# Kernel optimization log

Measured on AMD Instinct MI355X. Metric: run time of the kernel, lower is better.

Reference implementation:

```python
import jax, jax.numpy as jnp
import numpy as np
from jax import lax

M_POINT = 1024
NSAMPLE = 16
GRASPNESS_THRESHOLD = 0.1
HMIN, HMAX = -0.02, 0.04  # cylinder height range (GraspNet CloudCrop)
RADII = (0.025, 0.05, 0.075, 0.1)
BIG = 1e10


def _fps(xyz, mask):
    """Masked furthest point sampling. xyz [N,3], mask [N] bool -> idx [M_POINT] int32.
    Masked-out points carry -BIG min-distance so they are never selected."""
    first = jnp.argmax(mask).astype(jnp.int32)  # first graspable point (ragged FPS start)
    dists = jnp.where(mask, BIG, -BIG)
    idxs = jnp.zeros((M_POINT,), jnp.int32).at[0].set(first)

    def body(i, carry):
        idxs, dists = carry
        last = xyz[idxs[i - 1]]
        d = jnp.sum((xyz - last) ** 2, axis=-1)
        dists = jnp.where(mask, jnp.minimum(dists, d), -BIG)
        nxt = jnp.argmax(dists).astype(jnp.int32)
        return idxs.at[i].set(nxt), dists

    idxs, _ = lax.fori_loop(1, M_POINT, body, (idxs, dists))
    return idxs


def _cylinder_crop(xyz_g, feat_g, rot, radius, w1, b1, w2, b2):
    """Cylinder query + group + shared MLP + maxpool.
    xyz_g [B,M,3], feat_g [B,M,C], rot [B,M,3,3] -> [B,M,256]."""
    B, M, _ = xyz_g.shape
    # offsets of candidate n relative to seed m, expressed in the seed's gripper frame
    diff = xyz_g[:, None, :, :] - xyz_g[:, :, None, :]          # [B,M(seed),M(cand),3]
    local = jnp.einsum('bmnj,bmji->bmni', diff, rot)            # rotate into approach frame
    along = local[..., 0]
    r2 = local[..., 1] ** 2 + local[..., 2] ** 2
    cond = (r2 < radius * radius) & (along > HMIN) & (along < HMAX)  # [B,M,M]
    # first NSAMPLE in-cylinder indices (ball-query semantics: pad with first hit)
    order = jnp.where(cond, jnp.arange(M)[None, None, :], M)
    sel = jnp.argsort(order, axis=-1)[..., :NSAMPLE].astype(jnp.int32)  # [B,M,NS]
    cnt = cond.sum(axis=-1)                                     # [B,M]
    fill = sel[..., :1]
    idx = jnp.where(jnp.arange(NSAMPLE)[None, None, :] < cnt[..., None], sel, fill)
    idx = jnp.where(cnt[..., None] > 0, idx, 0)
    grouped_xyz = jnp.take_along_axis(local, idx[..., None], axis=2) / radius  # [B,M,NS,3]
    grouped_feat = feat_g[jnp.arange(B)[:, None, None], idx]                    # [B,M,NS,C]
    g = jnp.concatenate([grouped_xyz, grouped_feat], axis=-1)                   # [B,M,NS,3+C]
    h = jax.nn.relu(jnp.einsum('bmnf,of->bmno', g, w1) + b1)
    h = jax.nn.relu(jnp.einsum('bmnf,of->bmno', h, w2) + b2)
    return h.max(axis=2)                                                        # [B,M,256]


def setup_inputs() -> dict:
    key = jax.random.key(0)
    ks = jax.random.split(key, 10)
    B, N, C = 4, 20000, 512
    return {
        'seed_xyz': jax.random.normal(ks[0], (B, N, 3), jnp.float32),
        'seed_features': jax.random.normal(ks[1], (B, C, N), jnp.float32),
        'objectness_score': jax.random.normal(ks[2], (B, 2, N), jnp.float32),
        'graspness_score': jax.random.uniform(ks[3], (B, N), jnp.float32),
        'grasp_top_views_rot': jax.random.normal(ks[4], (B, M_POINT, 3, 3), jnp.float32),
        'crop_w1': jax.random.normal(ks[5], (4, 256, 3 + C), jnp.float32) * 0.05,
        'crop_b1': jnp.zeros((4, 256), jnp.float32),
        'crop_w2': jax.random.normal(ks[6], (4, 256, 256), jnp.float32) * 0.05,
        'crop_b2': jnp.zeros((4, 256), jnp.float32),
        'fuse_w': jax.random.normal(ks[7], (256, 1024), jnp.float32) * 0.05,
        'fuse_b': jnp.zeros((256,), jnp.float32),
    }


def reference(seed_xyz, seed_features, objectness_score, graspness_score,
              grasp_top_views_rot, crop_w1, crop_b1, crop_w2, crop_b2,
              fuse_w, fuse_b):
    # graspable mask (per-point, data dependent)
    objectness_mask = jnp.argmax(objectness_score, axis=1) == 1       # [B,N]
    graspness_mask = graspness_score > GRASPNESS_THRESHOLD
    graspable_mask = objectness_mask & graspness_mask
    # masked FPS per sample, then gather
    idxs = jax.vmap(_fps)(seed_xyz, graspable_mask)                    # [B,M]
    xyz_g = jnp.take_along_axis(seed_xyz, idxs[:, :, None], axis=1)    # [B,M,3]
    feat = seed_features.transpose(0, 2, 1)                            # [B,N,C]
    feat_g = jnp.take_along_axis(feat, idxs[:, :, None], axis=1)       # [B,M,C]
    # multiscale cylinder crops
    feats = [_cylinder_crop(xyz_g, feat_g, grasp_top_views_rot, RADII[k],
                            crop_w1[k], crop_b1[k], crop_w2[k], crop_b2[k])
             for k in range(4)]
    cat = jnp.concatenate(feats, axis=-1)                              # [B,M,1024]
    fused = jnp.einsum('bmf,of->bom', cat, fuse_w) + fuse_b[None, :, None]  # [B,256,M]
    return fused
```

## Files before the change

### kernel.cpp

```cpp
#include <hip/hip_runtime.h>
#include <cstdint>
#include <cfloat>
#include <climits>

#define NPTS 20000
#define NB 4
#define MP 1024
#define CF 512
#define MAXCH 20
#define PFIX 10
#define KFAST 10240
#define NWORK 8
#define PPT 20

__constant__ float c_r2[4]  = { (float)(0.025*0.025), (float)(0.05*0.05),
                                (float)(0.075*0.075), (float)(0.1*0.1) };
__constant__ float c_rad[4] = { 0.025f, 0.05f, 0.075f, 0.1f };

#define DPP_XOR1   0xB1
#define DPP_XOR2   0x4E
#define DPP_HMIRR  0x141
#define DPP_MIRR   0x140
#define DPP_BC15   0x142
#define DPP_BC31   0x143

template<int CTRL>
__device__ __forceinline__ unsigned long long kmax_step(unsigned long long k)
{
    unsigned int lo = (unsigned int)k;
    unsigned int hi = (unsigned int)(k >> 32);
    unsigned int olo = (unsigned int)__builtin_amdgcn_update_dpp((int)lo, (int)lo, CTRL, 0xf, 0xf, false);
    unsigned int ohi = (unsigned int)__builtin_amdgcn_update_dpp((int)hi, (int)hi, CTRL, 0xf, 0xf, false);
    unsigned long long ok = ((unsigned long long)ohi << 32) | (unsigned long long)olo;
    return (ok > k) ? ok : k;
}

__global__ __launch_bounds__(1024, 4)
void k_fps(const float* __restrict__ xyz, const float* __restrict__ obj,
           const float* __restrict__ grasp, int* __restrict__ idxs,
           float* __restrict__ xyz_g,
           float* __restrict__ xc, float* __restrict__ yc,
           float* __restrict__ zc, int* __restrict__ ci)
{
    const int b = blockIdx.x;
    const int tid = threadIdx.x;
    const int lane = tid & 63, wid = tid >> 6;
    const float* xb  = xyz   + (size_t)b * NPTS * 3;
    const float* ob0 = obj   + (size_t)b * 2 * NPTS;
    const float* ob1 = ob0 + NPTS;
    const float* gb  = grasp + (size_t)b * NPTS;
    float* xcb = xc + (size_t)b * 20480;
    float* ycb = yc + (size_t)b * 20480;
    float* zcb = zc + (size_t)b * 20480;
    int*   cib = ci + (size_t)b * 20480;

    __shared__ float sXYZ[3 * KFAST];
    __shared__ int   s_sel[MP];
    __shared__ unsigned long long sKey[2][16];
    __shared__ int   sWaveCnt[16];
    float* sX = sXYZ;
    float* sY = sXYZ + KFAST;
    float* sZ = sXYZ + 2 * KFAST;

    int kbase = 0;
    for (int i = 0; i < MAXCH; ++i) {
        int n = i * MP + tid;
        bool msk = false; float x = 0.f, y = 0.f, z = 0.f;
        if (n < NPTS) {
            msk = (ob1[n] > ob0[n]) && (gb[n] > 0.1f);
            if (msk) { x = xb[n*3+0]; y = xb[n*3+1]; z = xb[n*3+2]; }
        }
        unsigned long long bal = __ballot(msk);
        if (lane == 0) sWaveCnt[wid] = __popcll(bal);
        __syncthreads();
        int pre = 0, tot = 0;
        for (int w = 0; w < 16; ++w) { int c = sWaveCnt[w]; tot += c; if (w < wid) pre += c; }
        if (msk) {
            int rank = kbase + pre + __popcll(bal & ((1ull << lane) - 1ull));
            xcb[rank] = x; ycb[rank] = y; zcb[rank] = z; cib[rank] = n;
            if (rank < KFAST) { sX[rank] = x; sY[rank] = y; sZ[rank] = z; }
        }
        kbase += tot;
        __syncthreads();
    }
    const int K = kbase;

    if (K == 0) {
        idxs[b*MP + tid] = 0;
        xyz_g[((size_t)b*MP + tid)*3 + 0] = xb[0];
        xyz_g[((size_t)b*MP + tid)*3 + 1] = xb[1];
        xyz_g[((size_t)b*MP + tid)*3 + 2] = xb[2];
        return;
    }

    if (K <= KFAST) {
        const bool work = (wid < NWORK);
        float px[PPT], py[PPT], pz[PPT], pd[PPT];
        if (work) {
#pragma unroll
            for (int i = 0; i < PPT; ++i) {
                int c = tid + (i << 9);
                bool v = c < K;
                px[i] = v ? sX[c] : 0.f;
                py[i] = v ? sY[c] : 0.f;
                pz[i] = v ? sZ[c] : 0.f;
                pd[i] = v ? 1e10f : -3.0e38f;
            }
        }
        float lx = sX[0], ly = sY[0], lz = sZ[0];
        if (tid == 0) s_sel[0] = 0;

        for (int it = 1; it < MP; ++it) {
            const int p = it & 1;
            if (work) {
                float bv = -3.4e38f; int bn = 0;
#pragma unroll
                for (int i = 0; i < PPT; ++i) {
                    float dx = px[i] - lx, dy = py[i] - ly, dz = pz[i] - lz;
                    float d = __fadd_rn(__fadd_rn(__fmul_rn(dx,dx), __fmul_rn(dy,dy)),
                                        __fmul_rn(dz,dz));
                    float nd = fminf(pd[i], d);
                    pd[i] = nd;
                    bool w = nd > bv;
                    bn = w ? (tid + (i << 9)) : bn;
                    bv = fmaxf(bv, nd);
                }
                unsigned int ob = __float_as_uint(bv);
                unsigned int ord = (ob & 0x80000000u) ? ~ob : (ob | 0x80000000u);
                unsigned long long key = ((unsigned long long)ord << 32)
                                       | (unsigned int)(~bn);
                key = kmax_step<DPP_XOR1 >(key);
                key = kmax_step<DPP_XOR2 >(key);
                key = kmax_step<DPP_HMIRR>(key);
                key = kmax_step<DPP_MIRR >(key);
                key = kmax_step<DPP_BC15 >(key);
                key = kmax_step<DPP_BC31 >(key);
                if (lane == 63) sKey[p][wid] = key;
            }
            __syncthreads();
            if (work) {
                unsigned long long k2 = sKey[p][lane & 7];
                k2 = kmax_step<DPP_XOR1 >(k2);
                k2 = kmax_step<DPP_XOR2 >(k2);
                k2 = kmax_step<DPP_HMIRR>(k2);
                int n = ~((unsigned int)k2);
                lx = sX[n]; ly = sY[n]; lz = sZ[n];
                if (tid == 0) s_sel[it] = n;
            }
        }
        __syncthreads();
        int nc = s_sel[tid];
        idxs[b*MP + tid] = cib[nc];
        xyz_g[((size_t)b*MP + tid)*3 + 0] = sX[nc];
        xyz_g[((size_t)b*MP + tid)*3 + 1] = sY[nc];
        xyz_g[((size_t)b*MP + tid)*3 + 2] = sZ[nc];
        return;
    }

    {
        float* fD = sXYZ;
        for (int c = tid; c < K; c += MP) fD[c] = 1e10f;
        float lx = xcb[0], ly = ycb[0], lz = zcb[0];
        if (tid == 0) s_sel[0] = 0;
        __syncthreads();
        for (int it = 1; it < MP; ++it) {
            float bv = -3.4e38f; int bn = 0;
            for (int c = tid; c < K; c += MP) {
                float dx = xcb[c] - lx, dy = ycb[c] - ly, dz = zcb[c] - lz;
                float d = __fadd_rn(__fadd_rn(__fmul_rn(dx,dx), __fmul_rn(dy,dy)),
                                    __fmul_rn(dz,dz));
                float nd = fminf(fD[c], d);
                fD[c] = nd;
                bool w = nd > bv;
                bn = w ? c : bn;
                bv = fmaxf(bv, nd);
            }
            unsigned int ob = __float_as_uint(bv);
            unsigned int ord = (ob & 0x80000000u) ? ~ob : (ob | 0x80000000u);
            unsigned long long key = ((unsigned long long)ord << 32)
                                   | (unsigned int)(~bn);
#pragma unroll
            for (int off = 1; off < 64; off <<= 1) {
                unsigned long long ok = __shfl_xor(key, off);
                key = (ok > key) ? ok : key;
            }
            int p = it & 1;
            if (lane == 0) sKey[p][wid] = key;
            __syncthreads();
            unsigned long long k2 = sKey[p][lane & 15];
#pragma unroll
            for (int off = 1; off < 16; off <<= 1) {
                unsigned long long ok = __shfl_xor(k2, off);
                k2 = (ok > k2) ? ok : k2;
            }
            int n = ~((unsigned int)k2);
            lx = xcb[n]; ly = ycb[n]; lz = zcb[n];
            if (tid == 0) s_sel[it] = n;
        }
        __syncthreads();
        int nc = s_sel[tid];
        idxs[b*MP + tid] = cib[nc];
        xyz_g[((size_t)b*MP + tid)*3 + 0] = xcb[nc];
        xyz_g[((size_t)b*MP + tid)*3 + 1] = ycb[nc];
        xyz_g[((size_t)b*MP + tid)*3 + 2] = zcb[nc];
    }
}

__global__ void k_gather_feat(const float* __restrict__ sf, const int* __restrict__ idxs,
                              float* __restrict__ feat_g)
{
    int bm = blockIdx.x;
    int b = bm >> 10;
    int n = idxs[bm];
    const float* src = sf + (size_t)b*CF*NPTS + n;
    float* dst = feat_g + (size_t)bm*CF;
    for (int c = threadIdx.x; c < CF; c += 256) dst[c] = src[(size_t)c * NPTS];
}

__global__ void k_prep(const float* __restrict__ w1, const float* __restrict__ w2,
                       float* __restrict__ w2t, float* __restrict__ w1x)
{
    int k = blockIdx.x, cb = blockIdx.y*32, ob = blockIdx.z*32;
    int tx = threadIdx.x & 31, ty = threadIdx.x >> 5;
    __shared__ float t[32][33];
    for (int r = ty; r < 32; r += 8)
        t[r][tx] = w2[((size_t)k*256 + ob + r)*256 + cb + tx];
    __syncthreads();
    for (int r = ty; r < 32; r += 8)
        w2t[((size_t)k*256 + cb + r)*256 + ob + tx] = t[tx][r];
    if (blockIdx.y == 0 && blockIdx.z == 0) {
        int o = threadIdx.x;
        for (int d = 0; d < 3; ++d)
            w1x[(k*3 + d)*256 + o] = w1[((size_t)k*256 + o)*515 + d];
    }
}

__global__ __launch_bounds__(256)
void k_f1(const float* __restrict__ feat_g, const float* __restrict__ w1,
          const float* __restrict__ b1, float* __restrict__ F1)
{
    const int rt = blockIdx.x * 64;
    const int ot = blockIdx.y * 64;
    const int k  = blockIdx.z;
    const int tid = threadIdx.x;
    __shared__ float As[16][68];
    __shared__ float Bs[16][68];
    const int lr = tid >> 2;
    const int lc = (tid & 3) * 4;
    const int tr = (tid & 15) * 4;
    const int tc = (tid >> 4) * 4;
    float acc[4][4] = {};
    for (int kk = 0; kk < CF; kk += 16) {
        const float* ap = feat_g + (size_t)(rt + lr)*CF + kk + lc;
        As[lc+0][lr] = ap[0]; As[lc+1][lr] = ap[1];
        As[lc+2][lr] = ap[2]; As[lc+3][lr] = ap[3];
        const float* bp = w1 + (size_t)(k*256 + ot + lr)*515 + 3 + kk + lc;
        Bs[lc+0][lr] = bp[0]; Bs[lc+1][lr] = bp[1];
        Bs[lc+2][lr] = bp[2]; Bs[lc+3][lr] = bp[3];
        __syncthreads();
#pragma unroll
        for (int cc = 0; cc < 16; ++cc) {
            float a0=As[cc][tr+0], a1=As[cc][tr+1], a2=As[cc][tr+2], a3=As[cc][tr+3];
            float q0=Bs[cc][tc+0], q1=Bs[cc][tc+1], q2=Bs[cc][tc+2], q3=Bs[cc][tc+3];
            acc[0][0]+=a0*q0; acc[0][1]+=a0*q1; acc[0][2]+=a0*q2; acc[0][3]+=a0*q3;
            acc[1][0]+=a1*q0; acc[1][1]+=a1*q1; acc[1][2]+=a1*q2; acc[1][3]+=a1*q3;
            acc[2][0]+=a2*q0; acc[2][1]+=a2*q1; acc[2][2]+=a2*q2; acc[2][3]+=a2*q3;
            acc[3][0]+=a3*q0; acc[3][1]+=a3*q1; acc[3][2]+=a3*q2; acc[3][3]+=a3*q3;
        }
        __syncthreads();
    }
#pragma unroll
    for (int i = 0; i < 4; ++i)
#pragma unroll
        for (int j = 0; j < 4; ++j)
            F1[((size_t)k*4096 + rt+tr+i)*256 + ot+tc+j] = acc[i][j] + b1[k*256 + ot+tc+j];
}

__global__ __launch_bounds__(1024)
void k_nbr(const float* __restrict__ xyz_g, const float* __restrict__ rot,
           int* __restrict__ sel, float* __restrict__ lxyz, int* __restrict__ cnt)
{
    const int bm = blockIdx.x;
    const int b = bm >> 10;
    const int tid = threadIdx.x;
    const int lane = tid & 63, wid = tid >> 6;
    __shared__ float sR[9], sC[3];
    __shared__ int   sSel[4][16];
    __shared__ float sL[4][16][3];
    __shared__ int   sW[16];
    __shared__ int   sCnt[4];
    __shared__ float sFb[3];
    if (tid < 9) sR[tid] = rot[(size_t)bm*9 + tid];
    if (tid < 3) sC[tid] = xyz_g[(size_t)bm*3 + tid];
    __syncthreads();
    float x = xyz_g[((size_t)b*MP + tid)*3 + 0];
    float y = xyz_g[((size_t)b*MP + tid)*3 + 1];
    float z = xyz_g[((size_t)b*MP + tid)*3 + 2];
    float dx = x - sC[0], dy = y - sC[1], dz = z - sC[2];
    float l0 = __fadd_rn(__fadd_rn(__fmul_rn(dx,sR[0]), __fmul_rn(dy,sR[3])), __fmul_rn(dz,sR[6]));
    float l1 = __fadd_rn(__fadd_rn(__fmul_rn(dx,sR[1]), __fmul_rn(dy,sR[4])), __fmul_rn(dz,sR[7]));
    float l2 = __fadd_rn(__fadd_rn(__fmul_rn(dx,sR[2]), __fmul_rn(dy,sR[5])), __fmul_rn(dz,sR[8]));
    float r2 = __fadd_rn(__fmul_rn(l1,l1), __fmul_rn(l2,l2));
    bool basec = (l0 > -0.02f) && (l0 < 0.04f);
    if (tid == 0) { sFb[0]=l0; sFb[1]=l1; sFb[2]=l2; }
    for (int k = 0; k < 4; ++k) {
        bool c = basec && (r2 < c_r2[k]);
        unsigned long long bal = __ballot(c);
        if (lane == 0) sW[wid] = __popcll(bal);
        __syncthreads();
        int pre = 0, tot = 0;
        for (int w = 0; w < 16; ++w) { int cw = sW[w]; tot += cw; if (w < wid) pre += cw; }
        int rank = pre + __popcll(bal & ((1ull << lane) - 1ull));
        if (c && rank < 16) {
            sSel[k][rank] = tid;
            sL[k][rank][0] = l0; sL[k][rank][1] = l1; sL[k][rank][2] = l2;
        }
        if (tid == 0) sCnt[k] = min(tot, 16);
        __syncthreads();
    }
    if (tid < 64) {
        int k = tid >> 4, j = tid & 15;
        int ck = sCnt[k];
        int src = (j < ck) ? j : 0;
        int v; float a0, a1, a2;
        if (ck > 0) { v = sSel[k][src]; a0=sL[k][src][0]; a1=sL[k][src][1]; a2=sL[k][src][2]; }
        else        { v = 0; a0=sFb[0]; a1=sFb[1]; a2=sFb[2]; }
        size_t off = ((size_t)bm*4 + k)*16 + j;
        sel[off] = v;
        lxyz[off*3+0]=a0; lxyz[off*3+1]=a1; lxyz[off*3+2]=a2;
        if (j == 0) cnt[bm*4 + k] = (ck > 0) ? ck : 1;
    }
}

__global__ __launch_bounds__(256)
void k_mlp(const float* __restrict__ F1, const float* __restrict__ w1x,
           const float* __restrict__ w2t, const float* __restrict__ b2,
           const int* __restrict__ sel, const float* __restrict__ lxyz,
           const int* __restrict__ cnt, float* __restrict__ cat)
{
    const int gid = blockIdx.x;
    const int k = gid & 3;
    const int g0 = (gid >> 2) * 4;
    const int o = threadIdx.x;
    __shared__ float h1s[64][256];
    int u0 = cnt[(g0+0)*4 + k], u1 = cnt[(g0+1)*4 + k],
        u2 = cnt[(g0+2)*4 + k], u3 = cnt[(g0+3)*4 + k];
    int off1 = u0, off2 = u0+u1, off3 = off2+u2, tot = off3+u3;
    const float wx0 = w1x[(k*3+0)*256 + o];
    const float wx1 = w1x[(k*3+1)*256 + o];
    const float wx2 = w1x[(k*3+2)*256 + o];
    const float rad = c_rad[k];
    const int bbase = (g0 >> 10) * MP;
    for (int r = 0; r < tot; ++r) {
        int t = (r >= off1) + (r >= off2) + (r >= off3);
        int toff = (t==0) ? 0 : ((t==1) ? off1 : ((t==2) ? off2 : off3));
        int j = r - toff;
        int bmk = (g0 + t)*4 + k;
        int n = sel[(size_t)bmk*16 + j];
        float lx = lxyz[((size_t)bmk*16 + j)*3 + 0];
        float ly = lxyz[((size_t)bmk*16 + j)*3 + 1];
        float lz = lxyz[((size_t)bmk*16 + j)*3 + 2];
        float v = F1[((size_t)k*4096 + bbase + n)*256 + o];
        v += (lx/rad)*wx0 + (ly/rad)*wx1 + (lz/rad)*wx2;
        h1s[r][o] = fmaxf(v, 0.f);
    }
    __syncthreads();
    const float b2v = b2[k*256 + o];
    float m0=0.f, m1=0.f, m2=0.f, m3=0.f;
    const float* w2c = w2t + (size_t)k*65536 + o;
    for (int base = 0; base < tot; base += 4) {
        int r0 = base;
        int r1 = min(base+1, tot-1);
        int r2 = min(base+2, tot-1);
        int r3 = min(base+3, tot-1);
        float a0=0.f, a1=0.f, a2=0.f, a3=0.f;
        for (int c = 0; c < 256; c += 4) {
            float wA = w2c[(c+0)*256], wB = w2c[(c+1)*256];
            float wC = w2c[(c+2)*256], wD = w2c[(c+3)*256];
            float4 h;
            h = *(const float4*)&h1s[r0][c]; a0 += h.x*wA + h.y*wB + h.z*wC + h.w*wD;
            h = *(const float4*)&h1s[r1][c]; a1 += h.x*wA + h.y*wB + h.z*wC + h.w*wD;
            h = *(const float4*)&h1s[r2][c]; a2 += h.x*wA + h.y*wB + h.z*wC + h.w*wD;
            h = *(const float4*)&h1s[r3][c]; a3 += h.x*wA + h.y*wB + h.z*wC + h.w*wD;
        }
#pragma unroll
        for (int q = 0; q < 4; ++q) {
            int r = base + q;
            if (r < tot) {
                float a = (q==0) ? a0 : ((q==1) ? a1 : ((q==2) ? a2 : a3));
                int t = (r >= off1) + (r >= off2) + (r >= off3);
                float val = fmaxf(a + b2v, 0.f);
                if      (t==0) m0 = fmaxf(m0, val);
                else if (t==1) m1 = fmaxf(m1, val);
                else if (t==2) m2 = fmaxf(m2, val);
                else           m3 = fmaxf(m3, val);
            }
        }
    }
    cat[(size_t)(g0+0)*1024 + k*256 + o] = m0;
    cat[(size_t)(g0+1)*1024 + k*256 + o] = m1;
    cat[(size_t)(g0+2)*1024 + k*256 + o] = m2;
    cat[(size_t)(g0+3)*1024 + k*256 + o] = m3;
}

__global__ void k_transpose(const float* __restrict__ cat, float* __restrict__ catT)
{
    int bt = blockIdx.x;
    int b = bt >> 10;
    int t2 = bt & 1023;
    int mi = (t2 >> 5) * 32, fi = (t2 & 31) * 32;
    int tx = threadIdx.x & 31, ty = threadIdx.x >> 5;
    __shared__ float t[32][33];
    const float* src = cat + (size_t)b * 1048576;
    float* dst = catT + (size_t)b * 1048576;
    for (int r = ty; r < 32; r += 8) t[r][tx] = src[(size_t)(mi + r)*1024 + fi + tx];
    __syncthreads();
    for (int r = ty; r < 32; r += 8) dst[(size_t)(fi + r)*1024 + mi + tx] = t[tx][r];
}

__global__ __launch_bounds__(256)
void k_fuse(const float* __restrict__ catT, const float* __restrict__ fw,
            const float* __restrict__ fb, float* __restrict__ out)
{
    const int o0 = blockIdx.x * 4;
    const int b = blockIdx.y;
    const int m = threadIdx.x * 4;
    const float* ct = catT + (size_t)b * 1048576 + m;
    float4 a0 = {0,0,0,0}, a1 = a0, a2 = a0, a3 = a0;
    for (int f = 0; f < 1024; ++f) {
        const float4 cv = *(const float4*)(ct + (size_t)f*1024);
        float w0 = fw[(size_t)(o0+0)*1024 + f];
        float w1 = fw[(size_t)(o0+1)*1024 + f];
        float w2 = fw[(size_t)(o0+2)*1024 + f];
        float w3 = fw[(size_t)(o0+3)*1024 + f];
        a0.x += cv.x*w0; a0.y += cv.y*w0; a0.z += cv.z*w0; a0.w += cv.w*w0;
        a1.x += cv.x*w1; a1.y += cv.y*w1; a1.z += cv.z*w1; a1.w += cv.w*w1;
        a2.x += cv.x*w2; a2.y += cv.y*w2; a2.z += cv.z*w2; a2.w += cv.w*w2;
        a3.x += cv.x*w3; a3.y += cv.y*w3; a3.z += cv.z*w3; a3.w += cv.w*w3;
    }
#pragma unroll
    for (int q = 0; q < 4; ++q) {
        float bb = fb[o0+q];
        float4 r = (q==0) ? a0 : ((q==1) ? a1 : ((q==2) ? a2 : a3));
        r.x += bb; r.y += bb; r.z += bb; r.w += bb;
        *(float4*)&out[((size_t)b*256 + o0 + q)*1024 + m] = r;
    }
}

extern "C" void kernel_launch(void* const* d_in, const int* in_sizes, int n_in,
                              void* d_out, int out_size, void* d_ws, size_t ws_size,
                              hipStream_t stream)
{
    const float* seed_xyz      = (const float*)d_in[0];
    const float* seed_features = (const float*)d_in[1];
    const float* objectness    = (const float*)d_in[2];
    const float* graspness     = (const float*)d_in[3];
    const float* rot           = (const float*)d_in[4];
    const float* w1            = (const float*)d_in[5];
    const float* b1            = (const float*)d_in[6];
    const float* w2            = (const float*)d_in[7];
    const float* b2            = (const float*)d_in[8];
    const float* fw            = (const float*)d_in[9];
    const float* fb            = (const float*)d_in[10];
    float* out = (float*)d_out;

    char* ws = (char*)d_ws;
    size_t off = 0;
    int*   idxs   = (int*)(ws + off);  off += 16u<<10;
    float* xyz_g  = (float*)(ws + off); off += 48u<<10;
    float* feat_g = (float*)(ws + off); off += 8u<<20;
    float* F1     = (float*)(ws + off); off += 16u<<20;
    float* w2t    = (float*)(ws + off); off += 1u<<20;
    float* w1x    = (float*)(ws + off); off += 64u<<10;
    int*   sel    = (int*)(ws + off);   off += 1u<<20;
    int*   cnt    = (int*)(ws + off);   off += 64u<<10;
    float* lxyz   = (float*)(ws + off); off += 3u<<20;
    float* cat    = (float*)(ws + off); off += 16u<<20;
    float* catT   = (float*)(ws + off); off += 16u<<20;

    float* xc = cat;
    float* yc = cat + 4*20480;
    float* zc = cat + 8*20480;
    int*   ci = (int*)(cat + 12*20480);

    k_fps<<<NB, 1024, 0, stream>>>(seed_xyz, objectness, graspness, idxs, xyz_g,
                                   xc, yc, zc, ci);
    k_prep<<<dim3(4,8,8), 256, 0, stream>>>(w1, w2, w2t, w1x);
    k_gather_feat<<<NB*MP, 256, 0, stream>>>(seed_features, idxs, feat_g);
    k_f1<<<dim3(64,4,4), 256, 0, stream>>>(feat_g, w1, b1, F1);
    k_nbr<<<NB*MP, 1024, 0, stream>>>(xyz_g, rot, sel, lxyz, cnt);
    k_mlp<<<4096, 256, 0, stream>>>(F1, w1x, w2t, b2, sel, lxyz, cnt, cat);
    k_transpose<<<4096, 256, 0, stream>>>(cat, catT);
    k_fuse<<<dim3(64,4), 256, 0, stream>>>(catT, fw, fb, out);
}
```

Baseline: 1.744 ms.

## Split FPS into compaction and 512-thread loop kernels with tree argmax

Separates the masked compaction from the furthest-point-sampling loop into two kernels, with the loop kernel using 512-thread blocks so the per-iteration barrier covers only the 8 working waves. The per-thread argmax over 20 points becomes a tree reduction to shorten the serial dependency chain. The fallback path also switches its shuffle reductions to DPP. The split adds a kernel launch and a reload of the compacted points from global memory into shared memory.

```diff
diff --git a/kernel.cpp b/kernel.cpp
--- a/kernel.cpp
+++ b/kernel.cpp
@@ -8,9 +8,7 @@
 #define MP 1024
 #define CF 512
 #define MAXCH 20
-#define PFIX 10
 #define KFAST 10240
-#define NWORK 8
 #define PPT 20
 
 __constant__ float c_r2[4]  = { (float)(0.025*0.025), (float)(0.05*0.05),
@@ -35,12 +33,12 @@
     return (ok > k) ? ok : k;
 }
 
-__global__ __launch_bounds__(1024, 4)
-void k_fps(const float* __restrict__ xyz, const float* __restrict__ obj,
-           const float* __restrict__ grasp, int* __restrict__ idxs,
-           float* __restrict__ xyz_g,
-           float* __restrict__ xc, float* __restrict__ yc,
-           float* __restrict__ zc, int* __restrict__ ci)
+__global__ __launch_bounds__(1024)
+void k_fps_compact(const float* __restrict__ xyz, const float* __restrict__ obj,
+                   const float* __restrict__ grasp,
+                   float* __restrict__ xc, float* __restrict__ yc,
+                   float* __restrict__ zc, int* __restrict__ ci,
+                   int* __restrict__ kv)
 {
     const int b = blockIdx.x;
     const int tid = threadIdx.x;
@@ -54,13 +52,7 @@
     float* zcb = zc + (size_t)b * 20480;
     int*   cib = ci + (size_t)b * 20480;
 
-    __shared__ float sXYZ[3 * KFAST];
-    __shared__ int   s_sel[MP];
-    __shared__ unsigned long long sKey[2][16];
-    __shared__ int   sWaveCnt[16];
-    float* sX = sXYZ;
-    float* sY = sXYZ + KFAST;
-    float* sZ = sXYZ + 2 * KFAST;
+    __shared__ int sWaveCnt[16];
 
     int kbase = 0;
     for (int i = 0; i < MAXCH; ++i) {
@@ -78,94 +70,136 @@
         if (msk) {
             int rank = kbase + pre + __popcll(bal & ((1ull << lane) - 1ull));
             xcb[rank] = x; ycb[rank] = y; zcb[rank] = z; cib[rank] = n;
-            if (rank < KFAST) { sX[rank] = x; sY[rank] = y; sZ[rank] = z; }
         }
         kbase += tot;
         __syncthreads();
     }
-    const int K = kbase;
+    if (tid == 0) kv[b] = kbase;
+}
+
+__global__ __launch_bounds__(512, 2)
+void k_fps_loop(const float* __restrict__ xyz, const int* __restrict__ kv,
+                const float* __restrict__ xc, const float* __restrict__ yc,
+                const float* __restrict__ zc, const int* __restrict__ ci,
+                int* __restrict__ idxs, float* __restrict__ xyz_g)
+{
+    const int b = blockIdx.x;
+    const int tid = threadIdx.x;
+    const int lane = tid & 63, wid = tid >> 6;
+    const float* xb  = xyz + (size_t)b * NPTS * 3;
+    const float* xcb = xc + (size_t)b * 20480;
+    const float* ycb = yc + (size_t)b * 20480;
+    const float* zcb = zc + (size_t)b * 20480;
+    const int*   cib = ci + (size_t)b * 20480;
+
+    __shared__ float sXYZ[3 * KFAST];
+    __shared__ int   s_sel[MP];
+    __shared__ unsigned long long sKy[2][8];
+    float* sX = sXYZ;
+    float* sY = sXYZ + KFAST;
+    float* sZ = sXYZ + 2 * KFAST;
+
+    const int K = kv[b];
 
     if (K == 0) {
-        idxs[b*MP + tid] = 0;
-        xyz_g[((size_t)b*MP + tid)*3 + 0] = xb[0];
-        xyz_g[((size_t)b*MP + tid)*3 + 1] = xb[1];
-        xyz_g[((size_t)b*MP + tid)*3 + 2] = xb[2];
+        for (int t = tid; t < MP; t += 512) {
+            idxs[b*MP + t] = 0;
+            xyz_g[((size_t)b*MP + t)*3 + 0] = xb[0];
+            xyz_g[((size_t)b*MP + t)*3 + 1] = xb[1];
+            xyz_g[((size_t)b*MP + t)*3 + 2] = xb[2];
+        }
         return;
     }
 
     if (K <= KFAST) {
-        const bool work = (wid < NWORK);
+        for (int c = tid; c < KFAST; c += 512) {
+            bool v = c < K;
+            sX[c] = v ? xcb[c] : 0.f;
+            sY[c] = v ? ycb[c] : 0.f;
+            sZ[c] = v ? zcb[c] : 0.f;
+        }
+        __syncthreads();
+
         float px[PPT], py[PPT], pz[PPT], pd[PPT];
-        if (work) {
-#pragma unroll
-            for (int i = 0; i < PPT; ++i) {
-                int c = tid + (i << 9);
-                bool v = c < K;
-                px[i] = v ? sX[c] : 0.f;
-                py[i] = v ? sY[c] : 0.f;
-                pz[i] = v ? sZ[c] : 0.f;
-                pd[i] = v ? 1e10f : -3.0e38f;
-            }
+#pragma unroll
+        for (int i = 0; i < PPT; ++i) {
+            int c = tid + (i << 9);
+            px[i] = sX[c]; py[i] = sY[c]; pz[i] = sZ[c];
+            pd[i] = (c < K) ? 1e10f : -3.0e38f;
         }
         float lx = sX[0], ly = sY[0], lz = sZ[0];
         if (tid == 0) s_sel[0] = 0;
 
         for (int it = 1; it < MP; ++it) {
             const int p = it & 1;
-            if (work) {
-                float bv = -3.4e38f; int bn = 0;
-#pragma unroll
-                for (int i = 0; i < PPT; ++i) {
-                    float dx = px[i] - lx, dy = py[i] - ly, dz = pz[i] - lz;
-                    float d = __fadd_rn(__fadd_rn(__fmul_rn(dx,dx), __fmul_rn(dy,dy)),
-                                        __fmul_rn(dz,dz));
-                    float nd = fminf(pd[i], d);
-                    pd[i] = nd;
-                    bool w = nd > bv;
-                    bn = w ? (tid + (i << 9)) : bn;
-                    bv = fmaxf(bv, nd);
-                }
-                unsigned int ob = __float_as_uint(bv);
-                unsigned int ord = (ob & 0x80000000u) ? ~ob : (ob | 0x80000000u);
-                unsigned long long key = ((unsigned long long)ord << 32)
-                                       | (unsigned int)(~bn);
-                key = kmax_step<DPP_XOR1 >(key);
-                key = kmax_step<DPP_XOR2 >(key);
-                key = kmax_step<DPP_HMIRR>(key);
-                key = kmax_step<DPP_MIRR >(key);
-                key = kmax_step<DPP_BC15 >(key);
-                key = kmax_step<DPP_BC31 >(key);
-                if (lane == 63) sKey[p][wid] = key;
+#pragma unroll
+            for (int i = 0; i < PPT; ++i) {
+                float dx = px[i] - lx, dy = py[i] - ly, dz = pz[i] - lz;
+                float d = __fadd_rn(__fadd_rn(__fmul_rn(dx,dx), __fmul_rn(dy,dy)),
+                                    __fmul_rn(dz,dz));
+                pd[i] = fminf(pd[i], d);
             }
+            float gv[5]; int gi[5];
+#pragma unroll
+            for (int g = 0; g < 5; ++g) {
+                const int i0 = g * 4;
+                bool t0 = pd[i0+1] > pd[i0+0];
+                float v01 = t0 ? pd[i0+1] : pd[i0+0];
+                int   i01 = t0 ? (i0+1) : (i0+0);
+                bool t1 = pd[i0+3] > pd[i0+2];
+                float v23 = t1 ? pd[i0+3] : pd[i0+2];
+                int   i23 = t1 ? (i0+3) : (i0+2);
+                bool t2 = v23 > v01;
+                gv[g] = t2 ? v23 : v01;
+                gi[g] = t2 ? i23 : i01;
+            }
+            bool tA = gv[1] > gv[0]; float vA = tA ? gv[1] : gv[0]; int iA = tA ? gi[1] : gi[0];
+            bool tB = gv[3] > gv[2]; float vB = tB ? gv[3] : gv[2]; int iB = tB ? gi[3] : gi[2];
+            bool tC = vB > vA;       float vC = tC ? vB : vA;       int iC = tC ? iB : iA;
+            bool tD = gv[4] > vC;    float bv = tD ? gv[4] : vC;    int bi = tD ? gi[4] : iC;
+            int bn = tid + (bi << 9);
+
+            unsigned int ob = __float_as_uint(bv);
+            unsigned int ord = (ob & 0x80000000u) ? ~ob : (ob | 0x80000000u);
+            unsigned long long key = ((unsigned long long)ord << 32)
+                                   | (unsigned int)(~bn);
+            key = kmax_step<DPP_XOR1 >(key);
+            key = kmax_step<DPP_XOR2 >(key);
+            key = kmax_step<DPP_HMIRR>(key);
+            key = kmax_step<DPP_MIRR >(key);
+            key = kmax_step<DPP_BC15 >(key);
+            key = kmax_step<DPP_BC31 >(key);
+            if (lane == 63) sKy[p][wid] = key;
             __syncthreads();
-            if (work) {
-                unsigned long long k2 = sKey[p][lane & 7];
-                k2 = kmax_step<DPP_XOR1 >(k2);
-                k2 = kmax_step<DPP_XOR2 >(k2);
-                k2 = kmax_step<DPP_HMIRR>(k2);
-                int n = ~((unsigned int)k2);
-                lx = sX[n]; ly = sY[n]; lz = sZ[n];
-                if (tid == 0) s_sel[it] = n;
-            }
-        }
-        __syncthreads();
-        int nc = s_sel[tid];
-        idxs[b*MP + tid] = cib[nc];
-        xyz_g[((size_t)b*MP + tid)*3 + 0] = sX[nc];
-        xyz_g[((size_t)b*MP + tid)*3 + 1] = sY[nc];
-        xyz_g[((size_t)b*MP + tid)*3 + 2] = sZ[nc];
+            unsigned long long k2 = sKy[p][lane & 7];
+            k2 = kmax_step<DPP_XOR1 >(k2);
+            k2 = kmax_step<DPP_XOR2 >(k2);
+            k2 = kmax_step<DPP_HMIRR>(k2);
+            int n = ~((unsigned int)k2);
+            lx = sX[n]; ly = sY[n]; lz = sZ[n];
+            if (tid == 0) s_sel[it] = n;
+        }
+        __syncthreads();
+        for (int t = tid; t < MP; t += 512) {
+            int nc = s_sel[t];
+            idxs[b*MP + t] = cib[nc];
+            xyz_g[((size_t)b*MP + t)*3 + 0] = sX[nc];
+            xyz_g[((size_t)b*MP + t)*3 + 1] = sY[nc];
+            xyz_g[((size_t)b*MP + t)*3 + 2] = sZ[nc];
+        }
         return;
     }
 
     {
         float* fD = sXYZ;
-        for (int c = tid; c < K; c += MP) fD[c] = 1e10f;
+        for (int c = tid; c < K; c += 512) fD[c] = 1e10f;
         float lx = xcb[0], ly = ycb[0], lz = zcb[0];
         if (tid == 0) s_sel[0] = 0;
         __syncthreads();
         for (int it = 1; it < MP; ++it) {
+            const int p = it & 1;
             float bv = -3.4e38f; int bn = 0;
-            for (int c = tid; c < K; c += MP) {
+            for (int c = tid; c < K; c += 512) {
                 float dx = xcb[c] - lx, dy = ycb[c] - ly, dz = zcb[c] - lz;
                 float d = __fadd_rn(__fadd_rn(__fmul_rn(dx,dx), __fmul_rn(dy,dy)),
                                     __fmul_rn(dz,dz));
@@ -179,30 +213,30 @@
             unsigned int ord = (ob & 0x80000000u) ? ~ob : (ob | 0x80000000u);
             unsigned long long key = ((unsigned long long)ord << 32)
                                    | (unsigned int)(~bn);
-#pragma unroll
-            for (int off = 1; off < 64; off <<= 1) {
-                unsigned long long ok = __shfl_xor(key, off);
-                key = (ok > key) ? ok : key;
-            }
-            int p = it & 1;
-            if (lane == 0) sKey[p][wid] = key;
+            key = kmax_step<DPP_XOR1 >(key);
+            key = kmax_step<DPP_XOR2 >(key);
+            key = kmax_step<DPP_HMIRR>(key);
+            key = kmax_step<DPP_MIRR >(key);
+            key = kmax_step<DPP_BC15 >(key);
+            key = kmax_step<DPP_BC31 >(key);
+            if (lane == 63) sKy[p][wid] = key;
             __syncthreads();
-            unsigned long long k2 = sKey[p][lane & 15];
-#pragma unroll
-            for (int off = 1; off < 16; off <<= 1) {
-                unsigned long long ok = __shfl_xor(k2, off);
-                k2 = (ok > k2) ? ok : k2;
-            }
+            unsigned long long k2 = sKy[p][lane & 7];
+            k2 = kmax_step<DPP_XOR1 >(k2);
+            k2 = kmax_step<DPP_XOR2 >(k2);
+            k2 = kmax_step<DPP_HMIRR>(k2);
             int n = ~((unsigned int)k2);
             lx = xcb[n]; ly = ycb[n]; lz = zcb[n];
             if (tid == 0) s_sel[it] = n;
         }
         __syncthreads();
-        int nc = s_sel[tid];
-        idxs[b*MP + tid] = cib[nc];
-        xyz_g[((size_t)b*MP + tid)*3 + 0] = xcb[nc];
-        xyz_g[((size_t)b*MP + tid)*3 + 1] = ycb[nc];
-        xyz_g[((size_t)b*MP + tid)*3 + 2] = zcb[nc];
+        for (int t = tid; t < MP; t += 512) {
+            int nc = s_sel[t];
+            idxs[b*MP + t] = cib[nc];
+            xyz_g[((size_t)b*MP + t)*3 + 0] = xcb[nc];
+            xyz_g[((size_t)b*MP + t)*3 + 1] = ycb[nc];
+            xyz_g[((size_t)b*MP + t)*3 + 2] = zcb[nc];
+        }
     }
 }
 
@@ -482,9 +516,11 @@
     float* yc = cat + 4*20480;
     float* zc = cat + 8*20480;
     int*   ci = (int*)(cat + 12*20480);
-
-    k_fps<<<NB, 1024, 0, stream>>>(seed_xyz, objectness, graspness, idxs, xyz_g,
-                                   xc, yc, zc, ci);
+    int*   kv = (int*)((char*)w1x + 32768);
+
+    k_fps_compact<<<NB, 1024, 0, stream>>>(seed_xyz, objectness, graspness,
+                                           xc, yc, zc, ci, kv);
+    k_fps_loop<<<NB, 512, 0, stream>>>(seed_xyz, kv, xc, yc, zc, ci, idxs, xyz_g);
     k_prep<<<dim3(4,8,8), 256, 0, stream>>>(w1, w2, w2t, w1x);
     k_gather_feat<<<NB*MP, 256, 0, stream>>>(seed_features, idxs, feat_g);
     k_f1<<<dim3(64,4,4), 256, 0, stream>>>(feat_g, w1, b1, F1);
```

Result: no change. 1.725 ms (-1.1%).
